# Kernel tuning notes

Measured on AMD Instinct MI355X. Metric: run time of the kernel, lower is better.

The kernel has to match this reference:

```python
import jax, jax.numpy as jnp
import numpy as np
import math

E, H, FFN, NQ = 1024, 16, 4096, 8
B, T = 2, 2048
EPS = 1e-5

def layernorm(x, g, b):
    mu = jnp.mean(x, axis=-1, keepdims=True)
    var = jnp.mean(jnp.square(x - mu), axis=-1, keepdims=True)
    return (x - mu) * jax.lax.rsqrt(var + EPS) * g + b

def setup_inputs() -> dict:
    key = jax.random.key(0)
    ks = jax.random.split(key, 8)
    x = jax.random.normal(ks[0], (B, T, E), dtype=jnp.float32)
    mask = jnp.ones((B, T, T), dtype=bool)
    # constant quantum measurement output: PauliZ expectations of a fixed
    # RandomLayer circuit applied to |0..0> (independent of the input tokens)
    q_out = jax.random.uniform(ks[1], (NQ,), minval=-1.0, maxval=1.0, dtype=jnp.float32)
    s1 = 1.0 / math.sqrt(NQ)
    w1 = jax.random.uniform(ks[2], (NQ, FFN), minval=-s1, maxval=s1, dtype=jnp.float32)
    b1 = jnp.zeros((FFN,), dtype=jnp.float32)
    s2 = 1.0 / math.sqrt(FFN)
    w2 = jax.random.uniform(ks[3], (FFN, E), minval=-s2, maxval=s2, dtype=jnp.float32)
    b2 = jnp.zeros((E,), dtype=jnp.float32)
    g1 = jnp.ones((E,), dtype=jnp.float32); be1 = jnp.zeros((E,), dtype=jnp.float32)
    g2 = jnp.ones((E,), dtype=jnp.float32); be2 = jnp.zeros((E,), dtype=jnp.float32)
    return dict(x=x, mask=mask, q_out=q_out, w1=w1, b1=b1, w2=w2, b2=b2,
                g1=g1, be1=be1, g2=g2, be2=be2)

def reference(x, mask, q_out, w1, b1, w2, b2, g1, be1, g2, be2):
    b, t, e = x.shape
    d_k = e // H
    # q = k = v = head-split x (module has no QKV projections)
    q = x.reshape(b, t, H, d_k).transpose(0, 2, 1, 3)  # [B,H,T,d_k]
    scores = jnp.einsum('bhqd,bhkd->bhqk', q, q) / math.sqrt(d_k)
    scores = jnp.where(mask[:, None, :, :], scores, -1e9)
    attn = jax.nn.softmax(scores, axis=-1)
    out = jnp.einsum('bhqk,bhkd->bhqd', attn, q)
    attn_out = out.transpose(0, 2, 1, 3).reshape(b, t, e)
    x1 = layernorm(x + attn_out, g1, be1)
    # quantum FFN: constant measurement vector broadcast over all tokens
    h = jnp.broadcast_to(q_out, (b, t, NQ))
    h = jnp.dot(h, w1) + b1
    ffn_out = jnp.dot(jax.nn.relu(h), w2) + b2
    return layernorm(x1 + ffn_out, g2, be2)
```

## Files before the change

kernel.cpp:

```cpp
#include <hip/hip_runtime.h>

#define E_   1024
#define H_   16
#define DK_  64
#define FFN_ 4096
#define NQ_  8
#define B_   2
#define T_   2048
#define QBLK 64
#define KVBLK 64
#define NT_  (T_ / KVBLK)

#define NPART 256
#define ROWS_PER_PART (FFN_ / NPART)

typedef __attribute__((ext_vector_type(8))) __bf16 bf16x8;
typedef __attribute__((ext_vector_type(4))) float f32x4;

__device__ __forceinline__ __bf16 tobf(float f) { return (__bf16)f; }

__device__ __forceinline__ unsigned pk2(float a, float b) {
  union { __bf16 h; unsigned short u; } ua, ub;
  ua.h = (__bf16)a; ub.h = (__bf16)b;
  return (unsigned)ua.u | ((unsigned)ub.u << 16);
}

__global__ __launch_bounds__(256)
void cvt_kernel(const float* __restrict__ x, __bf16* __restrict__ xbf) {
  const size_t base = ((size_t)blockIdx.x * 256 + threadIdx.x) * 8;
  float4 a = *reinterpret_cast<const float4*>(x + base);
  float4 b = *reinterpret_cast<const float4*>(x + base + 4);
  bf16x8 v;
  v[0] = tobf(a.x); v[1] = tobf(a.y); v[2] = tobf(a.z); v[3] = tobf(a.w);
  v[4] = tobf(b.x); v[5] = tobf(b.y); v[6] = tobf(b.z); v[7] = tobf(b.w);
  *reinterpret_cast<bf16x8*>(xbf + base) = v;
}

__global__ __launch_bounds__(256)
void ffn_part_kernel(const float* __restrict__ q_out, const float* __restrict__ w1,
                     const float* __restrict__ b1, const float* __restrict__ w2,
                     float* __restrict__ part) {
  __shared__ float h[ROWS_PER_PART];
  const int tid = threadIdx.x;
  const int p = blockIdx.x;
  const int f0 = p * ROWS_PER_PART;
  if (tid < ROWS_PER_PART) {
    const int f = f0 + tid;
    float a = b1[f];
#pragma unroll
    for (int n = 0; n < NQ_; ++n) a += q_out[n] * w1[n * FFN_ + f];
    h[tid] = fmaxf(a, 0.f);
  }
  __syncthreads();
  float4 acc = {0.f, 0.f, 0.f, 0.f};
#pragma unroll
  for (int j = 0; j < ROWS_PER_PART; ++j) {
    const float hf = h[j];
    float4 w = reinterpret_cast<const float4*>(w2 + (size_t)(f0 + j) * E_)[tid];
    acc.x += hf * w.x; acc.y += hf * w.y; acc.z += hf * w.z; acc.w += hf * w.w;
  }
  reinterpret_cast<float4*>(part + (size_t)p * E_)[tid] = acc;
}

__global__ __launch_bounds__(256)
void ffn_reduce_kernel(const float* __restrict__ part, const float* __restrict__ b2,
                       float* __restrict__ ffn_c) {
  const int e = blockIdx.x * 256 + threadIdx.x;
  float a = b2[e];
  for (int r = 0; r < NPART; ++r) a += part[(size_t)r * E_ + e];
  ffn_c[e] = a;
}

__global__ __launch_bounds__(256)
void attn_kernel(const __bf16* __restrict__ xbf, float* __restrict__ out) {
  __shared__ __bf16 Kt[KVBLK][DK_ + 8];
  __shared__ __bf16 VtF[DK_ * KVBLK];
  __shared__ __bf16 Pl[4][16][DK_ + 8];

  const int tid  = threadIdx.x;
  const int wave = tid >> 6;
  const int lane = tid & 63;
  const int l16  = lane & 15;
  const int lhi  = lane >> 4;

  const int bh = blockIdx.y;
  const int b  = bh >> 4;
  const int h  = bh & 15;
  const int qbase = blockIdx.x * QBLK;
  const __bf16* xb = xbf + (size_t)b * T_ * E_ + h * DK_;

  bf16x8 qa[2];
  {
    const __bf16 sc = (__bf16)0.125f;
    const __bf16* qrow = xb + (size_t)(qbase + wave * 16 + l16) * E_;
    bf16x8 v0 = *reinterpret_cast<const bf16x8*>(qrow + lhi * 8);
    bf16x8 v1 = *reinterpret_cast<const bf16x8*>(qrow + 32 + lhi * 8);
#pragma unroll
    for (int j = 0; j < 8; ++j) { v0[j] *= sc; v1[j] *= sc; }
    qa[0] = v0; qa[1] = v1;
  }

  f32x4 acc[4];
#pragma unroll
  for (int td = 0; td < 4; ++td) acc[td] = (f32x4){0.f, 0.f, 0.f, 0.f};
  float lg = 0.f;

  const int kp = tid >> 3;
  const int d0 = (tid & 7) * 8;
  const __bf16* kvbase = xb + (size_t)(2 * kp) * E_ + d0;

  uint4 pr0 = *reinterpret_cast<const uint4*>(kvbase);
  uint4 pr1 = *reinterpret_cast<const uint4*>(kvbase + E_);

  for (int t = 0; t < NT_; ++t) {
    __syncthreads();
    {
      *reinterpret_cast<uint4*>(&Kt[2 * kp][d0])     = pr0;
      *reinterpret_cast<uint4*>(&Kt[2 * kp + 1][d0]) = pr1;
      union U4 { uint4 v; unsigned short s[8]; } u0, u1;
      u0.v = pr0; u1.v = pr1;
#pragma unroll
      for (int j = 0; j < 8; ++j) {
        const int d = d0 + j;
        const unsigned w = (unsigned)u0.s[j] | ((unsigned)u1.s[j] << 16);
        const int byte = d * 128 + ((4 * kp) ^ ((((d & 7) ^ ((d >> 3) & 7))) << 4));
        *reinterpret_cast<unsigned*>(reinterpret_cast<char*>(VtF) + byte) = w;
      }
    }
    if (t + 1 < NT_) {
      const __bf16* nb = kvbase + (size_t)(t + 1) * KVBLK * E_;
      pr0 = *reinterpret_cast<const uint4*>(nb);
      pr1 = *reinterpret_cast<const uint4*>(nb + E_);
    }
    __syncthreads();

    f32x4 s[4];
#pragma unroll
    for (int tn = 0; tn < 4; ++tn) {
      bf16x8 ka0 = *reinterpret_cast<const bf16x8*>(&Kt[tn * 16 + l16][lhi * 8]);
      bf16x8 ka1 = *reinterpret_cast<const bf16x8*>(&Kt[tn * 16 + l16][32 + lhi * 8]);
      f32x4 c = (f32x4){0.f, 0.f, 0.f, 0.f};
      c = __builtin_amdgcn_mfma_f32_16x16x32_bf16(ka0, qa[0], c, 0, 0, 0);
      c = __builtin_amdgcn_mfma_f32_16x16x32_bf16(ka1, qa[1], c, 0, 0, 0);
      s[tn] = c;
    }

#pragma unroll
    for (int tn = 0; tn < 4; ++tn) {
      float p0 = __expf(s[tn][0]), p1 = __expf(s[tn][1]);
      float p2 = __expf(s[tn][2]), p3 = __expf(s[tn][3]);
      lg += (p0 + p1) + (p2 + p3);
      uint2 w; w.x = pk2(p0, p1); w.y = pk2(p2, p3);
      *reinterpret_cast<uint2*>(&Pl[wave][l16][tn * 16 + lhi * 4]) = w;
    }
    asm volatile("s_waitcnt lgkmcnt(0)" ::: "memory");

#pragma unroll
    for (int kb = 0; kb < 2; ++kb) {
      bf16x8 pa = *reinterpret_cast<const bf16x8*>(&Pl[wave][l16][kb * 32 + lhi * 8]);
#pragma unroll
      for (int td = 0; td < 4; ++td) {
        const int d = td * 16 + l16;
        const int byte = d * 128 +
                         ((kb * 64 + lhi * 16) ^ (((d & 7) ^ ((d >> 3) & 7)) << 4));
        bf16x8 vb = *reinterpret_cast<const bf16x8*>(
            reinterpret_cast<const char*>(VtF) + byte);
        acc[td] = __builtin_amdgcn_mfma_f32_16x16x32_bf16(pa, vb, acc[td], 0, 0, 0);
      }
    }
  }

  lg += __shfl_xor(lg, 16); lg += __shfl_xor(lg, 32);
  float inv[4];
#pragma unroll
  for (int i = 0; i < 4; ++i) inv[i] = 1.f / __shfl(lg, lhi * 4 + i);
#pragma unroll
  for (int td = 0; td < 4; ++td)
#pragma unroll
    for (int i = 0; i < 4; ++i) {
      const int col = h * DK_ + td * 16 + l16;
      const size_t r0 = (size_t)b * T_ + qbase + wave * 16 + lhi * 4 + i;
      out[r0 * E_ + col] = acc[td][i] * inv[i];
    }
}

__device__ __forceinline__ float block_sum(float v, float* redrow, int lane, int wave) {
#pragma unroll
  for (int off = 1; off < 64; off <<= 1) v += __shfl_xor(v, off);
  if (lane == 0) redrow[wave] = v;
  __syncthreads();
  return redrow[0] + redrow[1] + redrow[2] + redrow[3];
}

__global__ __launch_bounds__(256)
void ln_kernel(const float* __restrict__ x, const float* __restrict__ ffn_c,
               const float* __restrict__ g1, const float* __restrict__ be1,
               const float* __restrict__ g2, const float* __restrict__ be2,
               float* io) {
  __shared__ float red[4][4];
  const int row = blockIdx.x;
  const int tid = threadIdx.x;
  const int lane = tid & 63, wave = tid >> 6;
  const float* xr = x + (size_t)row * E_;
  float* ior = io + (size_t)row * E_;

  float4 xv = reinterpret_cast<const float4*>(xr)[tid];
  float4 av = reinterpret_cast<const float4*>(ior)[tid];
  float v[4] = {xv.x + av.x, xv.y + av.y, xv.z + av.z, xv.w + av.w};

  float mu1 = block_sum(v[0] + v[1] + v[2] + v[3], red[0], lane, wave) * (1.f / E_);
  float q1 = 0.f;
#pragma unroll
  for (int j = 0; j < 4; ++j) { float d = v[j] - mu1; q1 += d * d; }
  float var1 = block_sum(q1, red[1], lane, wave) * (1.f / E_);
  float rs1 = rsqrtf(var1 + 1e-5f);

  const int e0 = tid * 4;
  float y[4];
#pragma unroll
  for (int j = 0; j < 4; ++j)
    y[j] = (v[j] - mu1) * rs1 * g1[e0 + j] + be1[e0 + j] + ffn_c[e0 + j];

  float mu2 = block_sum(y[0] + y[1] + y[2] + y[3], red[2], lane, wave) * (1.f / E_);
  float q2 = 0.f;
#pragma unroll
  for (int j = 0; j < 4; ++j) { float d = y[j] - mu2; q2 += d * d; }
  float var2 = block_sum(q2, red[3], lane, wave) * (1.f / E_);
  float rs2 = rsqrtf(var2 + 1e-5f);

  float4 o;
  o.x = (y[0] - mu2) * rs2 * g2[e0 + 0] + be2[e0 + 0];
  o.y = (y[1] - mu2) * rs2 * g2[e0 + 1] + be2[e0 + 1];
  o.z = (y[2] - mu2) * rs2 * g2[e0 + 2] + be2[e0 + 2];
  o.w = (y[3] - mu2) * rs2 * g2[e0 + 3] + be2[e0 + 3];
  reinterpret_cast<float4*>(ior)[tid] = o;
}

extern "C" void kernel_launch(void* const* d_in, const int* in_sizes, int n_in,
                              void* d_out, int out_size, void* d_ws, size_t ws_size,
                              hipStream_t stream) {
  (void)in_sizes; (void)n_in; (void)out_size; (void)ws_size;
  const float* x     = (const float*)d_in[0];
  const float* q_out = (const float*)d_in[2];
  const float* w1    = (const float*)d_in[3];
  const float* b1    = (const float*)d_in[4];
  const float* w2    = (const float*)d_in[5];
  const float* b2    = (const float*)d_in[6];
  const float* g1    = (const float*)d_in[7];
  const float* be1   = (const float*)d_in[8];
  const float* g2    = (const float*)d_in[9];
  const float* be2   = (const float*)d_in[10];
  float* out   = (float*)d_out;
  float* ffn_c = (float*)d_ws;
  float* part  = (float*)d_ws + E_;
  __bf16* xbf  = (__bf16*)((float*)d_ws + E_ + NPART * E_);

  cvt_kernel<<<(B_ * T_ * E_) / (256 * 8), 256, 0, stream>>>(x, xbf);
  ffn_part_kernel<<<NPART, 256, 0, stream>>>(q_out, w1, b1, w2, part);
  ffn_reduce_kernel<<<E_ / 256, 256, 0, stream>>>(part, b2, ffn_c);
  dim3 ag(T_ / QBLK, B_ * H_);
  attn_kernel<<<ag, 256, 0, stream>>>(xbf, out);
  ln_kernel<<<B_ * T_, 256, 0, stream>>>(x, ffn_c, g1, be1, g2, be2, out);
}
```

Measured before the change: 101.8 us.

## Load K fragments directly from global and double-buffer V tile to drop a barrier

The K tile is no longer staged in shared memory. Each wave loads its MFMA K fragments straight from global memory (L2/L1) into registers. The transposed V tile is double-buffered in LDS, which lets the loop-top __syncthreads be removed and saves LDS traffic. In exchange, every wave now reloads the same K rows from global memory, and the register load goes up.

```diff
diff --git a/kernel.cpp b/kernel.cpp
--- a/kernel.cpp
+++ b/kernel.cpp
@@ -73,8 +73,7 @@
 
 __global__ __launch_bounds__(256)
 void attn_kernel(const __bf16* __restrict__ xbf, float* __restrict__ out) {
-  __shared__ __bf16 Kt[KVBLK][DK_ + 8];
-  __shared__ __bf16 VtF[DK_ * KVBLK];
+  __shared__ __bf16 VtF[2][DK_ * KVBLK];
   __shared__ __bf16 Pl[4][16][DK_ + 8];
 
   const int tid  = threadIdx.x;
@@ -105,6 +104,8 @@
   for (int td = 0; td < 4; ++td) acc[td] = (f32x4){0.f, 0.f, 0.f, 0.f};
   float lg = 0.f;
 
+  const __bf16* xk = xb + (size_t)l16 * E_ + lhi * 8;
+
   const int kp = tid >> 3;
   const int d0 = (tid & 7) * 8;
   const __bf16* kvbase = xb + (size_t)(2 * kp) * E_ + d0;
@@ -113,18 +114,24 @@
   uint4 pr1 = *reinterpret_cast<const uint4*>(kvbase + E_);
 
   for (int t = 0; t < NT_; ++t) {
-    __syncthreads();
+    const int cur = t & 1;
+    bf16x8 kf[4][2];
+#pragma unroll
+    for (int tn = 0; tn < 4; ++tn) {
+      const __bf16* kt = xk + (size_t)(t * KVBLK + tn * 16) * E_;
+      kf[tn][0] = *reinterpret_cast<const bf16x8*>(kt);
+      kf[tn][1] = *reinterpret_cast<const bf16x8*>(kt + 32);
+    }
     {
-      *reinterpret_cast<uint4*>(&Kt[2 * kp][d0])     = pr0;
-      *reinterpret_cast<uint4*>(&Kt[2 * kp + 1][d0]) = pr1;
       union U4 { uint4 v; unsigned short s[8]; } u0, u1;
       u0.v = pr0; u1.v = pr1;
+      char* vb = reinterpret_cast<char*>(&VtF[cur][0]);
 #pragma unroll
       for (int j = 0; j < 8; ++j) {
         const int d = d0 + j;
         const unsigned w = (unsigned)u0.s[j] | ((unsigned)u1.s[j] << 16);
         const int byte = d * 128 + ((4 * kp) ^ ((((d & 7) ^ ((d >> 3) & 7))) << 4));
-        *reinterpret_cast<unsigned*>(reinterpret_cast<char*>(VtF) + byte) = w;
+        *reinterpret_cast<unsigned*>(vb + byte) = w;
       }
     }
     if (t + 1 < NT_) {
@@ -137,11 +144,9 @@
     f32x4 s[4];
 #pragma unroll
     for (int tn = 0; tn < 4; ++tn) {
-      bf16x8 ka0 = *reinterpret_cast<const bf16x8*>(&Kt[tn * 16 + l16][lhi * 8]);
-      bf16x8 ka1 = *reinterpret_cast<const bf16x8*>(&Kt[tn * 16 + l16][32 + lhi * 8]);
       f32x4 c = (f32x4){0.f, 0.f, 0.f, 0.f};
-      c = __builtin_amdgcn_mfma_f32_16x16x32_bf16(ka0, qa[0], c, 0, 0, 0);
-      c = __builtin_amdgcn_mfma_f32_16x16x32_bf16(ka1, qa[1], c, 0, 0, 0);
+      c = __builtin_amdgcn_mfma_f32_16x16x32_bf16(kf[tn][0], qa[0], c, 0, 0, 0);
+      c = __builtin_amdgcn_mfma_f32_16x16x32_bf16(kf[tn][1], qa[1], c, 0, 0, 0);
       s[tn] = c;
     }
 
@@ -163,9 +168,9 @@
         const int d = td * 16 + l16;
         const int byte = d * 128 +
                          ((kb * 64 + lhi * 16) ^ (((d & 7) ^ ((d >> 3) & 7)) << 4));
-        bf16x8 vb = *reinterpret_cast<const bf16x8*>(
-            reinterpret_cast<const char*>(VtF) + byte);
-        acc[td] = __builtin_amdgcn_mfma_f32_16x16x32_bf16(pa, vb, acc[td], 0, 0, 0);
+        bf16x8 vv = *reinterpret_cast<const bf16x8*>(
+            reinterpret_cast<const char*>(&VtF[cur][0]) + byte);
+        acc[td] = __builtin_amdgcn_mfma_f32_16x16x32_bf16(pa, vv, acc[td], 0, 0, 0);
       }
     }
   }
```

Result: slower. 164.1 us (+61.2%).
